# Performance work log

Hardware: AMD Instinct MI355X
Metric: run time of the kernel (lower is better)

Reference implementation:

```python
import jax, jax.numpy as jnp
import numpy as np

EPS = 1e-5

def layer_norm(x, gamma, beta):
    m = x.mean(axis=-1, keepdims=True)
    v = ((x - m) ** 2).mean(axis=-1, keepdims=True)  # correction=0
    return (x - m) / jnp.sqrt(v + EPS) * gamma + beta

def setup_inputs() -> dict:
    key = jax.random.key(0)
    B, T, E, H = 2, 2048, 1024, 16
    hd = E // H
    dff = 4 * E
    ks = jax.random.split(key, 10)
    s = 0.02
    return {
        "x": jax.random.normal(ks[0], (B, T, E), jnp.float32),
        "wq": jax.random.normal(ks[1], (H, E, hd), jnp.float32) * s,
        "wk": jax.random.normal(ks[2], (H, E, hd), jnp.float32) * s,
        "wv": jax.random.normal(ks[3], (H, E, hd), jnp.float32) * s,
        "w_proj": jax.random.normal(ks[4], (E, E), jnp.float32) * s,
        "b_proj": jnp.zeros((E,), jnp.float32),
        "gamma1": jnp.ones((E,), jnp.float32),
        "beta1": jnp.zeros((E,), jnp.float32),
        "gamma2": jnp.ones((E,), jnp.float32),
        "beta2": jnp.zeros((E,), jnp.float32),
        "w1": jax.random.normal(ks[5], (E, dff), jnp.float32) * s,
        "b1": jnp.zeros((dff,), jnp.float32),
        "w2": jax.random.normal(ks[6], (dff, E), jnp.float32) * s,
        "b2": jnp.zeros((E,), jnp.float32),
    }

def reference(x, wq, wk, wv, w_proj, b_proj, gamma1, beta1, gamma2, beta2, w1, b1, w2, b2):
    B, T, E = x.shape
    H, _, hd = wq.shape
    # pre-attention norm; NOTE: residual uses the normalized value (as in source)
    h = layer_norm(x, gamma1, beta1)
    # per-head projections, vectorized over heads: [B,H,T,hd]
    q = jnp.einsum('bte,hek->bhtk', h, wq)
    k = jnp.einsum('bte,hek->bhtk', h, wk)
    v = jnp.einsum('bte,hek->bhtk', h, wv)
    att = jnp.einsum('bhtk,bhsk->bhts', q, k) / jnp.sqrt(jnp.float32(hd))
    causal = jnp.tril(jnp.ones((T, T), bool))
    att = jnp.where(causal, att, -jnp.inf)
    p = jax.nn.softmax(att, axis=-1)  # dropout is identity in eval
    o = jnp.einsum('bhts,bhsk->bhtk', p, v)
    o = o.transpose(0, 2, 1, 3).reshape(B, T, E)  # concat heads
    attn_out = o @ w_proj + b_proj
    x2 = h + attn_out
    # pre-FFN norm; residual again uses normalized value
    h2 = layer_norm(x2, gamma2, beta2)
    ffn = jax.nn.relu(h2 @ w1 + b1) @ w2 + b2
    return h2 + ffn
```

## Files before the change

kernel.cpp:

```cpp
#include <hip/hip_runtime.h>
#include <stdint.h>

typedef unsigned short u16;
typedef __attribute__((ext_vector_type(8))) short short8;
typedef __attribute__((ext_vector_type(4))) short short4_t;
typedef __attribute__((ext_vector_type(4))) float f32x4;

__device__ __forceinline__ float b2f(u16 u){ union{unsigned i; float f;}v; v.i=((unsigned)u)<<16; return v.f; }
__device__ __forceinline__ u16 f2b(float f){ unsigned x=__float_as_uint(f); return (u16)((x + 0x7fffu + ((x>>16)&1u))>>16); }

#if __has_builtin(__builtin_amdgcn_exp2f)
#define EXP2F(x) __builtin_amdgcn_exp2f(x)
#else
#define EXP2F(x) exp2f(x)
#endif

__device__ __forceinline__ void async16(const void* g, void* l){
  __builtin_amdgcn_global_load_lds((const __attribute__((address_space(1))) void*)g,
                                   (__attribute__((address_space(3))) void*)l, 16, 0, 0);
}

template<int IN_F32>
__global__ __launch_bounds__(256) void ln_kernel(const void* __restrict__ xin,
    const float* __restrict__ g, const float* __restrict__ b, u16* __restrict__ y)
{
  const int E = 1024;
  int row = blockIdx.x, t = threadIdx.x;
  float f0,f1,f2,f3;
  if (IN_F32){
    const float* xr = (const float*)xin + (size_t)row*E;
    float4 xv = *(const float4*)(xr + t*4);
    f0=xv.x; f1=xv.y; f2=xv.z; f3=xv.w;
  } else {
    const u16* xr = (const u16*)xin + (size_t)row*E;
    ushort4 xv = *(const ushort4*)(xr + t*4);
    f0=b2f(xv.x); f1=b2f(xv.y); f2=b2f(xv.z); f3=b2f(xv.w);
  }
  float s1 = f0+f1+f2+f3;
  float s2 = f0*f0+f1*f1+f2*f2+f3*f3;
  #pragma unroll
  for (int off=32; off>=1; off>>=1){ s1 += __shfl_xor(s1,off); s2 += __shfl_xor(s2,off); }
  __shared__ float red[8];
  int w = t>>6;
  if ((t&63)==0){ red[w]=s1; red[4+w]=s2; }
  __syncthreads();
  float S1 = red[0]+red[1]+red[2]+red[3];
  float S2 = red[4]+red[5]+red[6]+red[7];
  float mean = S1*(1.0f/E);
  float var  = S2*(1.0f/E) - mean*mean;
  float inv  = rsqrtf(var + 1e-5f);
  float4 gv = *(const float4*)(g + t*4);
  float4 bv = *(const float4*)(b + t*4);
  ushort4 o;
  o.x = f2b((f0-mean)*inv*gv.x+bv.x);
  o.y = f2b((f1-mean)*inv*gv.y+bv.y);
  o.z = f2b((f2-mean)*inv*gv.z+bv.z);
  o.w = f2b((f3-mean)*inv*gv.w+bv.w);
  *(ushort4*)(y + (size_t)row*E + t*4) = o;
}

__global__ __launch_bounds__(256) void transpose_bt(const float* __restrict__ src, u16* __restrict__ dst,
                                                    int ld_src, int ld_dst)
{
  __shared__ u16 tile[64*66];
  int c0 = blockIdx.x*64, r0 = blockIdx.y*64;
  int t = threadIdx.x;
  #pragma unroll
  for (int i=0;i<16;++i){
    int lin = i*256 + t;
    int rr = lin>>6, cc = lin&63;
    tile[cc*66+rr] = f2b(src[(size_t)(r0+rr)*ld_src + c0+cc]);
  }
  __syncthreads();
  #pragma unroll
  for (int i=0;i<16;++i){
    int lin = i*256 + t;
    int cc = lin>>6, rr = lin&63;
    dst[(size_t)(c0+cc)*ld_dst + r0+rr] = tile[cc*66+rr];
  }
}

__global__ __launch_bounds__(256) void qkv_repack(const float* __restrict__ wq, const float* __restrict__ wk,
                                                  const float* __restrict__ wv, u16* __restrict__ dst)
{
  __shared__ u16 tile[64*66];
  int e0 = blockIdx.x*64;
  int sel = blockIdx.y>>4, h = blockIdx.y&15;
  const float* src = (sel==0?wq:(sel==1?wk:wv)) + (size_t)h*1024*64;
  int t = threadIdx.x;
  #pragma unroll
  for (int i=0;i<16;++i){
    int lin=i*256+t; int rr=lin>>6, cc=lin&63;
    tile[cc*66+rr] = f2b(src[(size_t)(e0+rr)*64 + cc]);
  }
  __syncthreads();
  #pragma unroll
  for (int i=0;i<16;++i){
    int lin=i*256+t; int cc=lin>>6, rr=lin&63;
    dst[(size_t)(sel*1024 + h*64 + cc)*1024 + e0+rr] = tile[cc*66+rr];
  }
}

__global__ __launch_bounds__(256) void vtrans(const u16* __restrict__ qkv, u16* __restrict__ VT)
{
  __shared__ u16 tile[64*66];
  int bh = blockIdx.y, bb = bh>>4, h = bh&15;
  int s0 = blockIdx.x*64;
  const u16* src = qkv + ((size_t)(bb*2048) + s0)*3072 + 2048 + h*64;
  int t = threadIdx.x;
  int sr = t>>3, c0 = (t&7)*8;
  #pragma unroll
  for (int half=0; half<2; ++half){
    const u16* p = src + (size_t)(sr+half*32)*3072 + c0;
    ushort4 v0 = *(const ushort4*)p;
    ushort4 v1 = *(const ushort4*)(p+4);
    uint* d = (uint*)(tile + (sr+half*32)*66 + c0);
    d[0] = (uint)v0.x | ((uint)v0.y<<16);
    d[1] = (uint)v0.z | ((uint)v0.w<<16);
    d[2] = (uint)v1.x | ((uint)v1.y<<16);
    d[3] = (uint)v1.z | ((uint)v1.w<<16);
  }
  __syncthreads();
  u16* out = VT + (size_t)bh*64*2048 + s0;
  int dw = t>>3, sc = (t&7)*8;
  #pragma unroll
  for (int half=0; half<2; ++half){
    int d = dw + half*32;
    short8 pk;
    #pragma unroll
    for (int j=0;j<8;++j) pk[j] = (short)tile[(sc+j)*66 + d];
    *(short8*)(out + (size_t)d*2048 + sc) = pk;
  }
}

template<int MI>
__global__ __launch_bounds__(256, 3) void gemm_bt(const u16* __restrict__ A, const u16* __restrict__ Bt,
    u16* __restrict__ C, float* __restrict__ Cf, int M, int N, int K,
    const float* __restrict__ bias, const u16* __restrict__ residual, int do_relu, int gx)
{
  __shared__ __align__(16) u16 As[2][MI*32*64];
  __shared__ __align__(16) u16 Bs[2][128*64];
  int t = threadIdx.x;
  int bid = blockIdx.y * gridDim.x + blockIdx.x;
  int xcd = bid & 7, slot = bid >> 3;
  int gy = 8 / gx;
  int rx = gridDim.x / gx, ry = gridDim.y / gy;
  int col_b = (xcd % gx) * rx + (slot % rx);
  int row_b = (xcd / gx) * ry + (slot / rx);
  int row0 = row_b*(MI*32), col0 = col_b*128;
  int l = t&63, w = t>>6;
  int wm = (w>>1)*(MI*16), wn = (w&1)*64;
  int lr = l&15, lq = l>>4;
  (void)M;

  f32x4 acc[MI][4];
  #pragma unroll
  for (int i=0;i<MI;++i)
    #pragma unroll
    for (int j=0;j<4;++j) acc[i][j] = f32x4{0.f,0.f,0.f,0.f};

  const u16* gA = A  + (size_t)(row0 + (t>>3))*K + (((t&7)^((t>>3)&7))<<3);
  const u16* gB = Bt + (size_t)(col0 + (t>>3))*K + (((t&7)^((t>>3)&7))<<3);
  const size_t rnd = (size_t)32*K;
  int nk = K>>6;

  #pragma unroll
  for (int r=0;r<MI;++r) async16(gA + r*rnd, As[0] + r*2048 + t*8);
  #pragma unroll
  for (int r=0;r<4;++r)  async16(gB + r*rnd, Bs[0] + r*2048 + t*8);

  int sw8 = (lr&7);
  for (int kt=0; kt<nk; ++kt){
    int cur = kt&1;
    __syncthreads();
    if (kt+1 < nk){
      int ko = (kt+1)<<6;
      #pragma unroll
      for (int r=0;r<MI;++r) async16(gA + r*rnd + ko, As[cur^1] + r*2048 + t*8);
      #pragma unroll
      for (int r=0;r<4;++r)  async16(gB + r*rnd + ko, Bs[cur^1] + r*2048 + t*8);
    }
    const u16* as = As[cur];
    const u16* bs = Bs[cur];
    #pragma unroll
    for (int kk=0;kk<2;++kk){
      int so = (((kk*4+lq)^sw8))<<3;
      short8 a[MI], b[4];
      #pragma unroll
      for (int i=0;i<MI;++i) a[i] = *(const short8*)(as + (wm+i*16+lr)*64 + so);
      #pragma unroll
      for (int j=0;j<4;++j)  b[j] = *(const short8*)(bs + (wn+j*16+lr)*64 + so);
      #pragma unroll
      for (int i=0;i<MI;++i)
        #pragma unroll
        for (int j=0;j<4;++j)
          acc[i][j] = __builtin_amdgcn_mfma_f32_16x16x32_bf16(a[i], b[j], acc[i][j], 0,0,0);
    }
  }

  #pragma unroll
  for (int i=0;i<MI;++i){
    #pragma unroll
    for (int j=0;j<4;++j){
      int col = col0 + wn + j*16 + lr;
      float bv = bias ? bias[col] : 0.0f;
      #pragma unroll
      for (int r=0;r<4;++r){
        int row = row0 + wm + i*16 + lq*4 + r;
        float v = acc[i][j][r] + bv;
        if (do_relu) v = fmaxf(v, 0.0f);
        if (residual) v += b2f(residual[(size_t)row*N + col]);
        if (Cf) Cf[(size_t)row*N + col] = v;
        else    C [(size_t)row*N + col] = f2b(v);
      }
    }
  }
}

__global__ __launch_bounds__(256) void attn_kernel(const u16* __restrict__ QKV,
    const u16* __restrict__ VT, u16* __restrict__ O)
{
  const int T=2048, LD=3072, E=1024;
  int bid = blockIdx.y * gridDim.x + blockIdx.x;
  int xcd = bid & 7, slot = bid >> 3;
  int qt = 15 - (slot & 15);
  int bh = xcd*4 + (slot >> 4);
  int bb = bh>>4, h = bh&15;
  int qbase = qt*128;
  const u16* base = QKV + (size_t)bb*T*LD;
  const u16* Qp = base + h*64;
  const u16* Kp = base + 1024 + h*64;
  const u16* Vtp = VT + (size_t)bh*64*2048;
  int t = threadIdx.x, l = t&63, w = t>>6;
  int lr = l&15, lq = l>>4;

  __shared__ __align__(16) u16 Ks[2][64*64];
  __shared__ __align__(16) u16 Vs[2][64*64];
  __shared__ __align__(16) u16 Pb[4][32*72];

  const float QSC = 0.125f*1.44269504f;
  short8 aq[2][2];
  #pragma unroll
  for (int qf=0;qf<2;++qf)
    #pragma unroll
    for (int kk=0;kk<2;++kk){
      const u16* qp = Qp + (size_t)(qbase + w*32 + qf*16 + lr)*LD + kk*32 + lq*8;
      short8 raw = *(const short8*)qp;
      short8 sc;
      #pragma unroll
      for (int j=0;j<8;++j) sc[j] = (short)f2b(b2f((u16)raw[j])*QSC);
      aq[qf][kk]=sc;
    }

  float mrun[2] = {-3e38f,-3e38f}, lrun[2] = {0.f,0.f};
  f32x4 Oacc[2][4];
  #pragma unroll
  for (int qf=0;qf<2;++qf)
    #pragma unroll
    for (int dt=0;dt<4;++dt) Oacc[qf][dt] = f32x4{0.f,0.f,0.f,0.f};

  int kc = (l&7) ^ (l>>3);
  int ra = 8*w + (l>>3);
  int qw0 = qbase + w*32;
  int nIter = 2*qt + 2;

  async16(Kp + (size_t)ra*LD      + kc*8, Ks[0] + ((size_t)w*64     + l)*8);
  async16(Kp + (size_t)(ra+32)*LD + kc*8, Ks[0] + ((size_t)(4+w)*64 + l)*8);
  async16(Vtp + (size_t)ra*2048      + kc*8, Vs[0] + ((size_t)w*64     + l)*8);
  async16(Vtp + (size_t)(ra+32)*2048 + kc*8, Vs[0] + ((size_t)(4+w)*64 + l)*8);

  for (int it=0; it<nIter; ++it){
    int s0 = it*64, cur = it&1;
    __syncthreads();
    if (it+1 < nIter){
      int sn = (it+1)*64;
      u16* kd = Ks[cur^1]; u16* vd = Vs[cur^1];
      async16(Kp + (size_t)(sn+ra)*LD      + kc*8, kd + ((size_t)w*64     + l)*8);
      async16(Kp + (size_t)(sn+ra+32)*LD   + kc*8, kd + ((size_t)(4+w)*64 + l)*8);
      async16(Vtp + (size_t)(ra)*2048    + sn + kc*8, vd + ((size_t)w*64     + l)*8);
      async16(Vtp + (size_t)(ra+32)*2048 + sn + kc*8, vd + ((size_t)(4+w)*64 + l)*8);
    }
    if (s0 <= qw0 + 31){
      const u16* ks = Ks[cur];
      const u16* vs = Vs[cur];
      bool need_mask = (s0 + 63 > qw0);
      f32x4 S[2][4];
      #pragma unroll
      for (int st=0; st<4; ++st){
        short8 kf0 = *(const short8*)(ks + (st*16+lr)*64 + ((lq  )^(lr&7))*8);
        short8 kf1 = *(const short8*)(ks + (st*16+lr)*64 + ((4+lq)^(lr&7))*8);
        #pragma unroll
        for (int qf=0;qf<2;++qf){
          f32x4 z = f32x4{0.f,0.f,0.f,0.f};
          z = __builtin_amdgcn_mfma_f32_16x16x32_bf16(kf0, aq[qf][0], z, 0,0,0);
          z = __builtin_amdgcn_mfma_f32_16x16x32_bf16(kf1, aq[qf][1], z, 0,0,0);
          S[qf][st] = z;
        }
      }
      if (need_mask){
        #pragma unroll
        for (int qf=0;qf<2;++qf){
          int qg = qw0 + qf*16 + lr;
          #pragma unroll
          for (int st=0;st<4;++st)
            #pragma unroll
            for (int r=0;r<4;++r){
              int sg = s0 + st*16 + lq*4 + r;
              if (sg > qg) S[qf][st][r] = -3e38f;
            }
        }
      }
      #pragma unroll
      for (int qf=0;qf<2;++qf){
        float m01 = fmaxf(fmaxf(S[qf][0][0],S[qf][0][1]),fmaxf(S[qf][0][2],S[qf][0][3]));
        float m11 = fmaxf(fmaxf(S[qf][1][0],S[qf][1][1]),fmaxf(S[qf][1][2],S[qf][1][3]));
        float m21 = fmaxf(fmaxf(S[qf][2][0],S[qf][2][1]),fmaxf(S[qf][2][2],S[qf][2][3]));
        float m31 = fmaxf(fmaxf(S[qf][3][0],S[qf][3][1]),fmaxf(S[qf][3][2],S[qf][3][3]));
        float m = fmaxf(fmaxf(m01,m11),fmaxf(m21,m31));
        m = fmaxf(m, __shfl_xor(m,16));
        m = fmaxf(m, __shfl_xor(m,32));
        float mnew = fmaxf(mrun[qf], m);
        float alpha = EXP2F(mrun[qf]-mnew);
        mrun[qf] = mnew;
        float ssum = 0.f;
        #pragma unroll
        for (int st=0;st<4;++st)
          #pragma unroll
          for (int r=0;r<4;++r){ float p = EXP2F(S[qf][st][r]-mnew); S[qf][st][r]=p; ssum+=p; }
        ssum += __shfl_xor(ssum,16);
        ssum += __shfl_xor(ssum,32);
        lrun[qf] = lrun[qf]*alpha + ssum;
        u16* pb = Pb[w] + (qf*16+lr)*72;
        #pragma unroll
        for (int st=0;st<4;++st){
          short4_t pk;
          pk.x=(short)f2b(S[qf][st][0]); pk.y=(short)f2b(S[qf][st][1]);
          pk.z=(short)f2b(S[qf][st][2]); pk.w=(short)f2b(S[qf][st][3]);
          *(short4_t*)(pb + st*16 + lq*4) = pk;
        }
        float af[4];
        #pragma unroll
        for (int r=0;r<4;++r) af[r] = __shfl(alpha, lq*4+r);
        #pragma unroll
        for (int dt=0;dt<4;++dt)
          #pragma unroll
          for (int r=0;r<4;++r) Oacc[qf][dt][r] *= af[r];
      }
      __asm__ volatile("s_waitcnt lgkmcnt(0)" ::: "memory");
      #pragma unroll
      for (int kk=0;kk<2;++kk){
        short8 pf0 = *(const short8*)(Pb[w] + (lr   )*72 + kk*32 + lq*8);
        short8 pf1 = *(const short8*)(Pb[w] + (16+lr)*72 + kk*32 + lq*8);
        #pragma unroll
        for (int dt=0;dt<4;++dt){
          short8 vf = *(const short8*)(vs + (dt*16+lr)*64 + (((kk*4+lq)^(lr&7)))*8);
          Oacc[0][dt] = __builtin_amdgcn_mfma_f32_16x16x32_bf16(pf0, vf, Oacc[0][dt], 0,0,0);
          Oacc[1][dt] = __builtin_amdgcn_mfma_f32_16x16x32_bf16(pf1, vf, Oacc[1][dt], 0,0,0);
        }
      }
    }
  }
  float linv[2][4];
  #pragma unroll
  for (int qf=0;qf<2;++qf)
    #pragma unroll
    for (int r=0;r<4;++r) linv[qf][r] = 1.0f/__shfl(lrun[qf], lq*4+r);
  #pragma unroll
  for (int qf=0;qf<2;++qf)
    #pragma unroll
    for (int dt=0;dt<4;++dt)
      #pragma unroll
      for (int r=0;r<4;++r){
        int qg = qbase + w*32 + qf*16 + lq*4 + r;
        O[(size_t)(bb*T+qg)*E + h*64 + dt*16 + lr] = f2b(Oacc[qf][dt][r]*linv[qf][r]);
      }
}

extern "C" void kernel_launch(void* const* d_in, const int* in_sizes, int n_in,
                              void* d_out, int out_size, void* d_ws, size_t ws_size,
                              hipStream_t stream)
{
  (void)in_sizes; (void)n_in; (void)out_size; (void)ws_size;
  const float* x     = (const float*)d_in[0];
  const float* wq    = (const float*)d_in[1];
  const float* wk    = (const float*)d_in[2];
  const float* wv    = (const float*)d_in[3];
  const float* wproj = (const float*)d_in[4];
  const float* bproj = (const float*)d_in[5];
  const float* g1    = (const float*)d_in[6];
  const float* be1   = (const float*)d_in[7];
  const float* g2    = (const float*)d_in[8];
  const float* be2   = (const float*)d_in[9];
  const float* w1    = (const float*)d_in[10];
  const float* b1    = (const float*)d_in[11];
  const float* w2    = (const float*)d_in[12];
  const float* b2    = (const float*)d_in[13];
  float* out = (float*)d_out;

  char* ws = (char*)d_ws;
  size_t off = 0;
  auto alloc = [&](size_t bytes)->void*{ void* p = ws + off; off += (bytes + 255) & ~(size_t)255; return p; };
  u16* hnorm  = (u16*)alloc((size_t)4096*1024*2);
  u16* qkv    = (u16*)alloc((size_t)4096*3072*2);
  u16* VT     = (u16*)alloc((size_t)32*64*2048*2);
  u16* attnO  = (u16*)alloc((size_t)4096*1024*2);
  u16* x2     = (u16*)alloc((size_t)4096*1024*2);
  u16* h2     = (u16*)alloc((size_t)4096*1024*2);
  u16* ffn1   = (u16*)alloc((size_t)4096*4096*2);
  u16* wqkvT  = (u16*)alloc((size_t)3072*1024*2);
  u16* wprojT = (u16*)alloc((size_t)1024*1024*2);
  u16* w1T    = (u16*)alloc((size_t)4096*1024*2);
  u16* w2T    = (u16*)alloc((size_t)1024*4096*2);

  qkv_repack  <<<dim3(16,48),256,0,stream>>>(wq,wk,wv,wqkvT);
  transpose_bt<<<dim3(16,16),256,0,stream>>>(wproj, wprojT, 1024, 1024);
  transpose_bt<<<dim3(64,16),256,0,stream>>>(w1,    w1T,    4096, 1024);
  transpose_bt<<<dim3(16,64),256,0,stream>>>(w2,    w2T,    1024, 4096);

  ln_kernel<1><<<4096,256,0,stream>>>(x, g1, be1, hnorm);
  gemm_bt<4><<<dim3(24,32),256,0,stream>>>(hnorm, wqkvT, qkv, nullptr, 4096,3072,1024, nullptr, nullptr, 0, 8);
  vtrans<<<dim3(32,32),256,0,stream>>>(qkv, VT);
  attn_kernel<<<dim3(16,32),256,0,stream>>>(qkv, VT, attnO);
  gemm_bt<2><<<dim3(8,64),256,0,stream>>>(attnO, wprojT, x2, nullptr, 4096,1024,1024, bproj, hnorm, 0, 2);
  ln_kernel<0><<<4096,256,0,stream>>>(x2, g2, be2, h2);
  gemm_bt<4><<<dim3(32,32),256,0,stream>>>(h2, w1T, ffn1, nullptr, 4096,4096,1024, b1, nullptr, 1, 8);
  gemm_bt<2><<<dim3(8,64),256,0,stream>>>(ffn1, w2T, nullptr, out, 4096,1024,4096, b2, h2, 0, 2);
}
```

Measured before the change: 400.1 us.

## Shrink attention query tile to 64 and keep P in registers via 16x16x16 MFMA

The attention kernel now gives each block a 64-row query tile, 16 rows per wave, instead of 128. The grid doubles to 1024 blocks, with a reworked XCD and causal load-balancing map that pairs long and short tiles. The P matrix is packed to bf16 in registers and fed directly to 16x16x16 MFMAs, which removes the per-wave LDS round trip and its waitcnt. Launch bounds request higher occupancy. In exchange, K/V tiles are reloaded from global memory twice as often, and the packing uses round-half-up instead of round-to-nearest-even.

Result: faster. 367.6 us (-8.1%).

```diff
diff --git a/kernel.cpp b/kernel.cpp
--- a/kernel.cpp
+++ b/kernel.cpp
@@ -15,9 +15,31 @@
 #define EXP2F(x) exp2f(x)
 #endif
 
+#if __has_builtin(__builtin_amdgcn_mfma_f32_16x16x16_bf16)
+#define MFMA16(a,b,c) __builtin_amdgcn_mfma_f32_16x16x16_bf16(a,b,c,0,0,0)
+#elif __has_builtin(__builtin_amdgcn_mfma_f32_16x16x16bf16_1k)
+#define MFMA16(a,b,c) __builtin_amdgcn_mfma_f32_16x16x16bf16_1k(a,b,c,0,0,0)
+#else
+static __device__ __forceinline__ f32x4 mfma16_asm(short4_t a, short4_t b, f32x4 c){
+  __asm__("v_mfma_f32_16x16x16_bf16 %0, %1, %2, %3" : "=v"(c) : "v"(a), "v"(b), "0"(c));
+  return c;
+}
+#define MFMA16(a,b,c) mfma16_asm(a,b,c)
+#endif
+
 __device__ __forceinline__ void async16(const void* g, void* l){
   __builtin_amdgcn_global_load_lds((const __attribute__((address_space(1))) void*)g,
                                    (__attribute__((address_space(3))) void*)l, 16, 0, 0);
+}
+
+__device__ __forceinline__ short4_t pack4(f32x4 s){
+  unsigned u0 = (__float_as_uint(s[0]) + 0x8000u) >> 16;
+  unsigned u1 = (__float_as_uint(s[1]) + 0x8000u) & 0xffff0000u;
+  unsigned u2 = (__float_as_uint(s[2]) + 0x8000u) >> 16;
+  unsigned u3 = (__float_as_uint(s[3]) + 0x8000u) & 0xffff0000u;
+  union { unsigned v[2]; short4_t s4; } r;
+  r.v[0] = u0 | u1; r.v[1] = u2 | u3;
+  return r.s4;
 }
 
 template<int IN_F32>
@@ -217,16 +239,16 @@
   }
 }
 
-__global__ __launch_bounds__(256) void attn_kernel(const u16* __restrict__ QKV,
+__global__ __launch_bounds__(256,4) void attn_kernel(const u16* __restrict__ QKV,
     const u16* __restrict__ VT, u16* __restrict__ O)
 {
   const int T=2048, LD=3072, E=1024;
   int bid = blockIdx.y * gridDim.x + blockIdx.x;
   int xcd = bid & 7, slot = bid >> 3;
-  int qt = 15 - (slot & 15);
-  int bh = xcd*4 + (slot >> 4);
+  int idx = slot & 31, grp = slot >> 5;
+  int qt = (grp & 1) ? idx : 31 - idx;
+  int bh = xcd*4 + grp;
   int bb = bh>>4, h = bh&15;
-  int qbase = qt*128;
   const u16* base = QKV + (size_t)bb*T*LD;
   const u16* Qp = base + h*64;
   const u16* Kp = base + 1024 + h*64;
@@ -236,144 +258,113 @@
 
   __shared__ __align__(16) u16 Ks[2][64*64];
   __shared__ __align__(16) u16 Vs[2][64*64];
-  __shared__ __align__(16) u16 Pb[4][32*72];
 
   const float QSC = 0.125f*1.44269504f;
-  short8 aq[2][2];
-  #pragma unroll
-  for (int qf=0;qf<2;++qf)
-    #pragma unroll
-    for (int kk=0;kk<2;++kk){
-      const u16* qp = Qp + (size_t)(qbase + w*32 + qf*16 + lr)*LD + kk*32 + lq*8;
-      short8 raw = *(const short8*)qp;
-      short8 sc;
-      #pragma unroll
-      for (int j=0;j<8;++j) sc[j] = (short)f2b(b2f((u16)raw[j])*QSC);
-      aq[qf][kk]=sc;
-    }
-
-  float mrun[2] = {-3e38f,-3e38f}, lrun[2] = {0.f,0.f};
-  f32x4 Oacc[2][4];
-  #pragma unroll
-  for (int qf=0;qf<2;++qf)
-    #pragma unroll
-    for (int dt=0;dt<4;++dt) Oacc[qf][dt] = f32x4{0.f,0.f,0.f,0.f};
+  int q0 = qt*64 + w*16;
+  short8 aq[2];
+  #pragma unroll
+  for (int kk=0;kk<2;++kk){
+    short8 raw = *(const short8*)(Qp + (size_t)(q0+lr)*LD + kk*32 + lq*8);
+    short8 sc;
+    #pragma unroll
+    for (int j=0;j<8;++j) sc[j] = (short)f2b(b2f((u16)raw[j])*QSC);
+    aq[kk]=sc;
+  }
+
+  float mrun = -3e38f, lrun = 0.f;
+  f32x4 Oacc[4];
+  #pragma unroll
+  for (int dt=0;dt<4;++dt) Oacc[dt] = f32x4{0.f,0.f,0.f,0.f};
 
   int kc = (l&7) ^ (l>>3);
   int ra = 8*w + (l>>3);
-  int qw0 = qbase + w*32;
-  int nIter = 2*qt + 2;
-
-  async16(Kp + (size_t)ra*LD      + kc*8, Ks[0] + ((size_t)w*64     + l)*8);
-  async16(Kp + (size_t)(ra+32)*LD + kc*8, Ks[0] + ((size_t)(4+w)*64 + l)*8);
-  async16(Vtp + (size_t)ra*2048      + kc*8, Vs[0] + ((size_t)w*64     + l)*8);
-  async16(Vtp + (size_t)(ra+32)*2048 + kc*8, Vs[0] + ((size_t)(4+w)*64 + l)*8);
-
-  for (int it=0; it<nIter; ++it){
+
+  async16(Kp  + (size_t)ra*LD        + kc*8, Ks[0] + t*8);
+  async16(Kp  + (size_t)(ra+32)*LD   + kc*8, Ks[0] + 2048 + t*8);
+  async16(Vtp + (size_t)ra*2048      + kc*8, Vs[0] + t*8);
+  async16(Vtp + (size_t)(ra+32)*2048 + kc*8, Vs[0] + 2048 + t*8);
+
+  for (int it=0; it<=qt; ++it){
     int s0 = it*64, cur = it&1;
     __syncthreads();
-    if (it+1 < nIter){
-      int sn = (it+1)*64;
+    if (it < qt){
+      int sn = s0+64;
       u16* kd = Ks[cur^1]; u16* vd = Vs[cur^1];
-      async16(Kp + (size_t)(sn+ra)*LD      + kc*8, kd + ((size_t)w*64     + l)*8);
-      async16(Kp + (size_t)(sn+ra+32)*LD   + kc*8, kd + ((size_t)(4+w)*64 + l)*8);
-      async16(Vtp + (size_t)(ra)*2048    + sn + kc*8, vd + ((size_t)w*64     + l)*8);
-      async16(Vtp + (size_t)(ra+32)*2048 + sn + kc*8, vd + ((size_t)(4+w)*64 + l)*8);
-    }
-    if (s0 <= qw0 + 31){
-      const u16* ks = Ks[cur];
-      const u16* vs = Vs[cur];
-      bool need_mask = (s0 + 63 > qw0);
-      f32x4 S[2][4];
-      #pragma unroll
-      for (int st=0; st<4; ++st){
-        short8 kf0 = *(const short8*)(ks + (st*16+lr)*64 + ((lq  )^(lr&7))*8);
-        short8 kf1 = *(const short8*)(ks + (st*16+lr)*64 + ((4+lq)^(lr&7))*8);
+      async16(Kp  + (size_t)(sn+ra)*LD        + kc*8, kd + t*8);
+      async16(Kp  + (size_t)(sn+ra+32)*LD     + kc*8, kd + 2048 + t*8);
+      async16(Vtp + (size_t)ra*2048      + sn + kc*8, vd + t*8);
+      async16(Vtp + (size_t)(ra+32)*2048 + sn + kc*8, vd + 2048 + t*8);
+    }
+    const u16* ks = Ks[cur];
+    const u16* vs = Vs[cur];
+
+    f32x4 S[4];
+    #pragma unroll
+    for (int st=0; st<4; ++st){
+      short8 kf0 = *(const short8*)(ks + (st*16+lr)*64 + ((lq  )^(lr&7))*8);
+      short8 kf1 = *(const short8*)(ks + (st*16+lr)*64 + ((4+lq)^(lr&7))*8);
+      f32x4 z = f32x4{0.f,0.f,0.f,0.f};
+      z = __builtin_amdgcn_mfma_f32_16x16x32_bf16(kf0, aq[0], z, 0,0,0);
+      z = __builtin_amdgcn_mfma_f32_16x16x32_bf16(kf1, aq[1], z, 0,0,0);
+      S[st] = z;
+    }
+    if (it == qt){
+      int qg = q0 + lr;
+      #pragma unroll
+      for (int st=0;st<4;++st)
         #pragma unroll
-        for (int qf=0;qf<2;++qf){
-          f32x4 z = f32x4{0.f,0.f,0.f,0.f};
-          z = __builtin_amdgcn_mfma_f32_16x16x32_bf16(kf0, aq[qf][0], z, 0,0,0);
-          z = __builtin_amdgcn_mfma_f32_16x16x32_bf16(kf1, aq[qf][1], z, 0,0,0);
-          S[qf][st] = z;
+        for (int r=0;r<4;++r){
+          int sg = s0 + st*16 + lq*4 + r;
+          if (sg > qg) S[st][r] = -3e38f;
         }
+    }
+    float m = S[0][0];
+    #pragma unroll
+    for (int st=0;st<4;++st)
+      #pragma unroll
+      for (int r=0;r<4;++r) m = fmaxf(m, S[st][r]);
+    m = fmaxf(m, __shfl_xor(m,16));
+    m = fmaxf(m, __shfl_xor(m,32));
+    float mnew = fmaxf(mrun, m);
+    float alpha = EXP2F(mrun - mnew);
+    mrun = mnew;
+    float ssum = 0.f;
+    #pragma unroll
+    for (int st=0;st<4;++st)
+      #pragma unroll
+      for (int r=0;r<4;++r){ float p = EXP2F(S[st][r]-mnew); S[st][r]=p; ssum+=p; }
+    ssum += __shfl_xor(ssum,16);
+    ssum += __shfl_xor(ssum,32);
+    lrun = lrun*alpha + ssum;
+    short4_t pk[4];
+    #pragma unroll
+    for (int st=0;st<4;++st) pk[st] = pack4(S[st]);
+    float af[4];
+    #pragma unroll
+    for (int r=0;r<4;++r) af[r] = __shfl(alpha, lq*4+r);
+    #pragma unroll
+    for (int dt=0;dt<4;++dt)
+      #pragma unroll
+      for (int r=0;r<4;++r) Oacc[dt][r] *= af[r];
+    #pragma unroll
+    for (int st=0;st<4;++st){
+      #pragma unroll
+      for (int dt=0;dt<4;++dt){
+        short4_t vf = *(const short4_t*)(vs + (dt*16+lr)*64 + ((2*st+(lq>>1))^(lr&7))*8 + (lq&1)*4);
+        Oacc[dt] = MFMA16(pk[st], vf, Oacc[dt]);
       }
-      if (need_mask){
-        #pragma unroll
-        for (int qf=0;qf<2;++qf){
-          int qg = qw0 + qf*16 + lr;
-          #pragma unroll
-          for (int st=0;st<4;++st)
-            #pragma unroll
-            for (int r=0;r<4;++r){
-              int sg = s0 + st*16 + lq*4 + r;
-              if (sg > qg) S[qf][st][r] = -3e38f;
-            }
-        }
-      }
-      #pragma unroll
-      for (int qf=0;qf<2;++qf){
-        float m01 = fmaxf(fmaxf(S[qf][0][0],S[qf][0][1]),fmaxf(S[qf][0][2],S[qf][0][3]));
-        float m11 = fmaxf(fmaxf(S[qf][1][0],S[qf][1][1]),fmaxf(S[qf][1][2],S[qf][1][3]));
-        float m21 = fmaxf(fmaxf(S[qf][2][0],S[qf][2][1]),fmaxf(S[qf][2][2],S[qf][2][3]));
-        float m31 = fmaxf(fmaxf(S[qf][3][0],S[qf][3][1]),fmaxf(S[qf][3][2],S[qf][3][3]));
-        float m = fmaxf(fmaxf(m01,m11),fmaxf(m21,m31));
-        m = fmaxf(m, __shfl_xor(m,16));
-        m = fmaxf(m, __shfl_xor(m,32));
-        float mnew = fmaxf(mrun[qf], m);
-        float alpha = EXP2F(mrun[qf]-mnew);
-        mrun[qf] = mnew;
-        float ssum = 0.f;
-        #pragma unroll
-        for (int st=0;st<4;++st)
-          #pragma unroll
-          for (int r=0;r<4;++r){ float p = EXP2F(S[qf][st][r]-mnew); S[qf][st][r]=p; ssum+=p; }
-        ssum += __shfl_xor(ssum,16);
-        ssum += __shfl_xor(ssum,32);
-        lrun[qf] = lrun[qf]*alpha + ssum;
-        u16* pb = Pb[w] + (qf*16+lr)*72;
-        #pragma unroll
-        for (int st=0;st<4;++st){
-          short4_t pk;
-          pk.x=(short)f2b(S[qf][st][0]); pk.y=(short)f2b(S[qf][st][1]);
-          pk.z=(short)f2b(S[qf][st][2]); pk.w=(short)f2b(S[qf][st][3]);
-          *(short4_t*)(pb + st*16 + lq*4) = pk;
-        }
-        float af[4];
-        #pragma unroll
-        for (int r=0;r<4;++r) af[r] = __shfl(alpha, lq*4+r);
-        #pragma unroll
-        for (int dt=0;dt<4;++dt)
-          #pragma unroll
-          for (int r=0;r<4;++r) Oacc[qf][dt][r] *= af[r];
-      }
-      __asm__ volatile("s_waitcnt lgkmcnt(0)" ::: "memory");
-      #pragma unroll
-      for (int kk=0;kk<2;++kk){
-        short8 pf0 = *(const short8*)(Pb[w] + (lr   )*72 + kk*32 + lq*8);
-        short8 pf1 = *(const short8*)(Pb[w] + (16+lr)*72 + kk*32 + lq*8);
-        #pragma unroll
-        for (int dt=0;dt<4;++dt){
-          short8 vf = *(const short8*)(vs + (dt*16+lr)*64 + (((kk*4+lq)^(lr&7)))*8);
-          Oacc[0][dt] = __builtin_amdgcn_mfma_f32_16x16x32_bf16(pf0, vf, Oacc[0][dt], 0,0,0);
-          Oacc[1][dt] = __builtin_amdgcn_mfma_f32_16x16x32_bf16(pf1, vf, Oacc[1][dt], 0,0,0);
-        }
-      }
-    }
-  }
-  float linv[2][4];
-  #pragma unroll
-  for (int qf=0;qf<2;++qf)
-    #pragma unroll
-    for (int r=0;r<4;++r) linv[qf][r] = 1.0f/__shfl(lrun[qf], lq*4+r);
-  #pragma unroll
-  for (int qf=0;qf<2;++qf)
-    #pragma unroll
-    for (int dt=0;dt<4;++dt)
-      #pragma unroll
-      for (int r=0;r<4;++r){
-        int qg = qbase + w*32 + qf*16 + lq*4 + r;
-        O[(size_t)(bb*T+qg)*E + h*64 + dt*16 + lr] = f2b(Oacc[qf][dt][r]*linv[qf][r]);
-      }
+    }
+  }
+  float linv[4];
+  #pragma unroll
+  for (int r=0;r<4;++r) linv[r] = 1.0f/__shfl(lrun, lq*4+r);
+  #pragma unroll
+  for (int dt=0;dt<4;++dt)
+    #pragma unroll
+    for (int r=0;r<4;++r){
+      int qg = q0 + lq*4 + r;
+      O[(size_t)(bb*T+qg)*E + h*64 + dt*16 + lr] = f2b(Oacc[dt][r]*linv[r]);
+    }
 }
 
 extern "C" void kernel_launch(void* const* d_in, const int* in_sizes, int n_in,
@@ -420,7 +411,7 @@
   ln_kernel<1><<<4096,256,0,stream>>>(x, g1, be1, hnorm);
   gemm_bt<4><<<dim3(24,32),256,0,stream>>>(hnorm, wqkvT, qkv, nullptr, 4096,3072,1024, nullptr, nullptr, 0, 8);
   vtrans<<<dim3(32,32),256,0,stream>>>(qkv, VT);
-  attn_kernel<<<dim3(16,32),256,0,stream>>>(qkv, VT, attnO);
+  attn_kernel<<<dim3(32,32),256,0,stream>>>(qkv, VT, attnO);
   gemm_bt<2><<<dim3(8,64),256,0,stream>>>(attnO, wprojT, x2, nullptr, 4096,1024,1024, bproj, hnorm, 0, 2);
   ln_kernel<0><<<4096,256,0,stream>>>(x2, g2, be2, h2);
   gemm_bt<4><<<dim3(32,32),256,0,stream>>>(h2, w1T, ffn1, nullptr, 4096,4096,1024, b1, nullptr, 1, 8);
```
